# Kernel optimization log

Measured on AMD Instinct MI355X. Metric: run time of the kernel, lower is better.

The kernel has to match this reference:

```python
import jax, jax.numpy as jnp
import numpy as np

N_NODES = 500_000
N_EDGES = 1_000_000
EMB = 64           # config.Model.embedding_size
F = 128            # config.Model.latency_feature_size
L = 8              # config.Latency.latency_feature_length
OP_CNT = 5000
SV_CNT = 2000
ST_CNT = 16
IN_DIM = 3 * EMB + L  # 200


def setup_inputs() -> dict:
    key = jax.random.key(0)
    ks = jax.random.split(key, 24)
    s = 0.02
    inp = {
        'operation_id': jax.random.randint(ks[0], (N_NODES,), 0, OP_CNT, dtype=jnp.int32),
        'service_id':   jax.random.randint(ks[1], (N_NODES,), 0, SV_CNT, dtype=jnp.int32),
        'status_id':    jax.random.randint(ks[2], (N_NODES,), 0, ST_CNT, dtype=jnp.int32),
        'latency_feat': jax.random.normal(ks[3], (N_NODES, L), dtype=jnp.float32),
        'edge_src':     jax.random.randint(ks[4], (N_EDGES,), 0, N_NODES, dtype=jnp.int32),
        'edge_dst':     jax.random.randint(ks[5], (N_EDGES,), 0, N_NODES, dtype=jnp.int32),
        'eps':          jax.random.normal(ks[6], (N_NODES, F), dtype=jnp.float32),
        # parameters (LevelEmbedding + TreeLSTMLatencyEncoder + TreeLSTMLatencyDecoder)
        'op_embed':      jax.random.normal(ks[7],  (OP_CNT, EMB), dtype=jnp.float32) * s,
        'service_embed': jax.random.normal(ks[8],  (SV_CNT, EMB), dtype=jnp.float32) * s,
        'status_embed':  jax.random.normal(ks[9],  (ST_CNT, EMB), dtype=jnp.float32) * s,
        'enc_W1': jax.random.normal(ks[10], (IN_DIM, F), dtype=jnp.float32) * s,
        'enc_b1': jnp.zeros((F,), dtype=jnp.float32),
        'enc_W2': jax.random.normal(ks[11], (F, 2 * F), dtype=jnp.float32) * s,
        'enc_b2': jnp.zeros((2 * F,), dtype=jnp.float32),
        'dec_Wself': jax.random.normal(ks[12], (F, F), dtype=jnp.float32) * s,
        'dec_Wagg':  jax.random.normal(ks[13], (F, F), dtype=jnp.float32) * s,
        'mu_W': jax.random.normal(ks[14], (F, L), dtype=jnp.float32) * s,
        'mu_b': jnp.zeros((L,), dtype=jnp.float32),
        'lv_W': jax.random.normal(ks[15], (F, L), dtype=jnp.float32) * s,
        'lv_b': jnp.zeros((L,), dtype=jnp.float32),
        'opwise_embed': jax.random.normal(ks[16], (OP_CNT + 1, 2 * L * L), dtype=jnp.float32) * s,
    }
    return inp


def reference(operation_id, service_id, status_id, latency_feat, edge_src, edge_dst, eps,
              op_embed, service_embed, status_embed,
              enc_W1, enc_b1, enc_W2, enc_b2,
              dec_Wself, dec_Wagg, mu_W, mu_b, lv_W, lv_b, opwise_embed):
    N = latency_feat.shape[0]
    # ---- LevelEmbedding: gathers + concat ----
    feats = jnp.concatenate([
        op_embed[operation_id],
        service_embed[service_id],
        status_embed[status_id],
        latency_feat,
    ], axis=-1)  # [N, 3*EMB + L]
    # ---- TreeLSTMLatencyEncoder ----
    h = jax.nn.relu(feats @ enc_W1 + enc_b1)
    y = h @ enc_W2 + enc_b2                       # [N, 2F]
    z_mu, z_lv = jnp.split(y, 2, axis=-1)
    z_lv = jnp.tanh(z_lv)
    z = z_mu + jnp.exp(0.5 * z_lv) * eps          # reparameterize, [N, F]
    # ---- TreeLSTM decoder (one child-sum message-passing step over edges) ----
    agg = jax.ops.segment_sum(z[edge_src], edge_dst, num_segments=N)  # scatter-reduce
    yd = jax.nn.relu(z @ dec_Wself + agg @ dec_Wagg)                  # [N, F]
    mu = yd @ mu_W + mu_b   # [N, L]
    lv = yd @ lv_W + lv_b   # [N, L]
    # op-wise output transform: per-node [1,L] @ [L,L]
    w = opwise_embed[operation_id].reshape(N, L, 2 * L)
    w_mu, w_lv = w[..., :L], w[..., L:]
    mu = jnp.einsum('nl,nlk->nk', mu, w_mu)
    lv = jnp.einsum('nl,nlk->nk', lv, w_lv)
    # ---- latency_loss: gaussian NLL + opid scatter aggregation ----
    label = latency_feat
    loss = (mu - label) ** 2 / (2.0 * jnp.exp(lv) + 1e-7) + 0.5 * lv  # [N, L]
    loss_node = jnp.mean(loss, axis=1)                                 # [N]
    op_loss = jax.ops.segment_sum(loss_node, operation_id, num_segments=OP_CNT)
    op_cnt = jax.ops.segment_sum(jnp.ones((N,), jnp.int32), operation_id, num_segments=OP_CNT)
    lat_loss = jnp.mean(loss_node)
    kl = -0.5 * jnp.mean(z_lv + 1.0 - jnp.exp(z_lv) - z_mu ** 2)
    total = lat_loss + kl
    return (total, op_loss, op_cnt)
```

## Files before the change

kernel.cpp:

```cpp
#include <hip/hip_runtime.h>
#include <math.h>

#define NN 500000
#define NE 1000000
#define OPC 5000
#define NBLK_SCAN 489
#define NBLK ((NN + 127) / 128)

typedef short short8 __attribute__((ext_vector_type(8)));
typedef float f32x4 __attribute__((ext_vector_type(4)));

static __device__ __forceinline__ short f2bf(float f) {
    unsigned u = __builtin_bit_cast(unsigned, f);
    u += 0x7fffu + ((u >> 16) & 1u);
    return (short)(u >> 16);
}
static __device__ __forceinline__ float bf2f(short s) {
    unsigned u = ((unsigned)(unsigned short)s) << 16;
    return __builtin_bit_cast(float, u);
}
static __device__ __forceinline__ short8 cvt8(float4 a, float4 b) {
    short8 r;
    r[0] = f2bf(a.x); r[1] = f2bf(a.y); r[2] = f2bf(a.z); r[3] = f2bf(a.w);
    r[4] = f2bf(b.x); r[5] = f2bf(b.y); r[6] = f2bf(b.z); r[7] = f2bf(b.w);
    return r;
}
static __device__ __forceinline__ short8 ldcvt(const float* p) {
    const float4* p4 = (const float4*)p;
    return cvt8(p4[0], p4[1]);
}

__global__ void prep_kernel(const float* __restrict__ W1, const float* __restrict__ W2,
                            const float* __restrict__ Wself, const float* __restrict__ Wagg,
                            const float* __restrict__ muW, const float* __restrict__ lvW,
                            short* __restrict__ W1f, short* __restrict__ W2f,
                            short* __restrict__ Wf0, short* __restrict__ Wf1,
                            short* __restrict__ HWf)
{
    int idx = blockIdx.x * 256 + threadIdx.x;
    int j = idx & 7, lane = (idx >> 3) & 63;
    int m = lane & 15, q = lane >> 4;
    {
        int s = idx >> 12, nf = (idx >> 9) & 7;
        int k = s * 32 + q * 8 + j, col = nf * 16 + m;
        W1f[idx] = (k < 200) ? f2bf(W1[k * 128 + col]) : (short)0;
    }
    {
        int s = idx >> 13, nf = (idx >> 9) & 15;
        int k = s * 32 + q * 8 + j, col = nf * 16 + m;
        W2f[idx] = f2bf(W2[k * 256 + col]);
    }
    if (idx < 16384) {
        int s = idx >> 12, nf = (idx >> 9) & 7;
        int k = s * 32 + q * 8 + j, col = nf * 16 + m;
        Wf0[idx] = f2bf(Wself[k * 128 + col]);
        Wf1[idx] = f2bf(Wagg[k * 128 + col]);
    }
    if (idx < 2048) {
        int k = (idx >> 9) * 32 + q * 8 + j;
        HWf[idx] = (m < 8) ? f2bf(muW[k * 8 + m]) : f2bf(lvW[k * 8 + (m - 8)]);
    }
}

__global__ __launch_bounds__(256, 4) void enc1_mfma(
    const int* __restrict__ op_id, const int* __restrict__ sv_id, const int* __restrict__ st_id,
    const float* __restrict__ lat,
    const float* __restrict__ opE, const float* __restrict__ svE, const float* __restrict__ stE,
    const short* __restrict__ W1f, const float* __restrict__ b1,
    short* __restrict__ h_bf)
{
    __shared__ __align__(16) short Hs[128 * 136];
    const int tid = threadIdx.x;
    const int lane = tid & 63, w = tid >> 6;
    const int m = lane & 15, q = lane >> 4;
    const int bbase = blockIdx.x * 128;
    const int wbase = bbase + w * 32;
    const bool wv = (wbase < NN);

    f32x4 acc[2][8];
    #pragma unroll
    for (int a2 = 0; a2 < 2; a2++)
        #pragma unroll
        for (int nf = 0; nf < 8; nf++) acc[a2][nf] = (f32x4)0.0f;

    if (wv) {
        const int n0 = wbase + m, n1 = wbase + 16 + m;
        const size_t op0 = (size_t)op_id[n0] * 64, op1 = (size_t)op_id[n1] * 64;
        const size_t sv0 = (size_t)sv_id[n0] * 64, sv1 = (size_t)sv_id[n1] * 64;
        const size_t st0 = (size_t)st_id[n0] * 64, st1 = (size_t)st_id[n1] * 64;

        #pragma unroll
        for (int s = 0; s < 7; s++) {
            short8 a0, a1;
            if (s < 2) {
                a0 = ldcvt(opE + op0 + s * 32 + q * 8);
                a1 = ldcvt(opE + op1 + s * 32 + q * 8);
            } else if (s < 4) {
                a0 = ldcvt(svE + sv0 + (s - 2) * 32 + q * 8);
                a1 = ldcvt(svE + sv1 + (s - 2) * 32 + q * 8);
            } else if (s < 6) {
                a0 = ldcvt(stE + st0 + (s - 4) * 32 + q * 8);
                a1 = ldcvt(stE + st1 + (s - 4) * 32 + q * 8);
            } else {
                if (q == 0) {
                    a0 = ldcvt(lat + (size_t)n0 * 8);
                    a1 = ldcvt(lat + (size_t)n1 * 8);
                } else {
                    #pragma unroll
                    for (int i = 0; i < 8; i++) { a0[i] = 0; a1[i] = 0; }
                }
            }
            #pragma unroll
            for (int nf = 0; nf < 8; nf++) {
                const short8 b = *(const short8*)(W1f + (s * 8 + nf) * 512 + lane * 8);
                acc[0][nf] = __builtin_amdgcn_mfma_f32_16x16x32_bf16(a0, b, acc[0][nf], 0, 0, 0);
                acc[1][nf] = __builtin_amdgcn_mfma_f32_16x16x32_bf16(a1, b, acc[1][nf], 0, 0, 0);
            }
        }
    }

    if (wv) {
        #pragma unroll
        for (int nf = 0; nf < 8; nf++) {
            int col = nf * 16 + m;
            float bb = b1[col];
            #pragma unroll
            for (int a2 = 0; a2 < 2; a2++)
                #pragma unroll
                for (int r = 0; r < 4; r++) {
                    int g = w * 32 + a2 * 16 + q * 4 + r;
                    Hs[g * 136 + col] = f2bf(fmaxf(acc[a2][nf][r] + bb, 0.0f));
                }
        }
    }
    __syncthreads();

    {
        int g = tid >> 1, cb = (tid & 1) * 64;
        int node = bbase + g;
        if (node < NN) {
            short8* dst = (short8*)(h_bf + (size_t)node * 128 + cb);
            const short8* src = (const short8*)&Hs[g * 136 + cb];
            #pragma unroll
            for (int i = 0; i < 8; i++) dst[i] = src[i];
        }
    }
}

__global__ __launch_bounds__(256, 4) void enc2_mfma(
    const short* __restrict__ h_bf, const short* __restrict__ W2f, const float* __restrict__ b2,
    const float* __restrict__ eps, short* __restrict__ z_bf, float* __restrict__ kl_sum)
{
    __shared__ __align__(16) int ldsI[64 * 132];
    const int tid = threadIdx.x;
    const int lane = tid & 63, w = tid >> 6;
    const int m = lane & 15, q = lane >> 4;
    const int bbase = blockIdx.x * 128;
    const int wbase = bbase + w * 32;
    const bool wv = (wbase < NN);

    f32x4 acc[2][16];
    #pragma unroll
    for (int a2 = 0; a2 < 2; a2++)
        #pragma unroll
        for (int nf = 0; nf < 16; nf++) acc[a2][nf] = (f32x4)0.0f;

    if (wv) {
        short8 a[2][4];
        #pragma unroll
        for (int s = 0; s < 4; s++) {
            a[0][s] = *(const short8*)(h_bf + (size_t)(wbase + m) * 128 + s * 32 + q * 8);
            a[1][s] = *(const short8*)(h_bf + (size_t)(wbase + 16 + m) * 128 + s * 32 + q * 8);
        }
        #pragma unroll
        for (int s = 0; s < 4; s++) {
            #pragma unroll
            for (int nf = 0; nf < 16; nf++) {
                const short8 b = *(const short8*)(W2f + (s * 16 + nf) * 512 + lane * 8);
                acc[0][nf] = __builtin_amdgcn_mfma_f32_16x16x32_bf16(a[0][s], b, acc[0][nf], 0, 0, 0);
                acc[1][nf] = __builtin_amdgcn_mfma_f32_16x16x32_bf16(a[1][s], b, acc[1][nf], 0, 0, 0);
            }
        }
    }

    float kll = 0.0f;
    #pragma unroll
    for (int a2 = 0; a2 < 2; a2++) {
        if (wv) {
            #pragma unroll
            for (int nf = 0; nf < 8; nf++) {
                int col = nf * 16 + m;
                float bm = b2[col], bl = b2[col + 128];
                #pragma unroll
                for (int r = 0; r < 4; r++) {
                    float mu = acc[a2][nf][r] + bm;
                    float lr = acc[a2][nf + 8][r] + bl;
                    float e2 = __expf(2.0f * lr);
                    float t  = 1.0f - 2.0f * __builtin_amdgcn_rcpf(e2 + 1.0f);
                    float s  = __expf(0.5f * t);
                    kll += t + 1.0f - s * s - mu * mu;
                    int pk = (int)(unsigned short)f2bf(mu)
                           | ((int)(unsigned short)f2bf(s) << 16);
                    ldsI[(w * 16 + q * 4 + r) * 132 + col] = pk;
                }
            }
        }
        __syncthreads();
        {
            int g = tid >> 2, cb = (tid & 3) * 32;
            int node = bbase + (g >> 4) * 32 + a2 * 16 + (g & 15);
            if (node < NN) {
                const float4* ep = (const float4*)(eps + (size_t)node * 128 + cb);
                const int4*   lp = (const int4*)&ldsI[g * 132 + cb];
                #pragma unroll
                for (int c = 0; c < 4; c++) {
                    int4 va = lp[c * 2], vb = lp[c * 2 + 1];
                    float4 ea = ep[c * 2], eb = ep[c * 2 + 1];
                    short8 o;
                    o[0] = f2bf(fmaf(bf2f((short)(va.x >> 16)), ea.x, bf2f((short)va.x)));
                    o[1] = f2bf(fmaf(bf2f((short)(va.y >> 16)), ea.y, bf2f((short)va.y)));
                    o[2] = f2bf(fmaf(bf2f((short)(va.z >> 16)), ea.z, bf2f((short)va.z)));
                    o[3] = f2bf(fmaf(bf2f((short)(va.w >> 16)), ea.w, bf2f((short)va.w)));
                    o[4] = f2bf(fmaf(bf2f((short)(vb.x >> 16)), eb.x, bf2f((short)vb.x)));
                    o[5] = f2bf(fmaf(bf2f((short)(vb.y >> 16)), eb.y, bf2f((short)vb.y)));
                    o[6] = f2bf(fmaf(bf2f((short)(vb.z >> 16)), eb.z, bf2f((short)vb.z)));
                    o[7] = f2bf(fmaf(bf2f((short)(vb.w >> 16)), eb.w, bf2f((short)vb.w)));
                    *(short8*)(z_bf + (size_t)node * 128 + cb + c * 8) = o;
                }
            }
        }
        __syncthreads();
    }
    #pragma unroll
    for (int off = 32; off > 0; off >>= 1) kll += __shfl_down(kll, off);
    if (lane == 0) atomicAdd(kl_sum, kll);
}

__global__ void hist_kernel(const int* __restrict__ edst, int* __restrict__ cnt)
{
    int e = blockIdx.x * 256 + threadIdx.x;
    if (e < NE) atomicAdd(&cnt[edst[e]], 1);
}

__global__ void scan1_kernel(const int* __restrict__ cnt, int* __restrict__ bsum)
{
    __shared__ int ls[256];
    int b = blockIdx.x, tid = threadIdx.x;
    int idx0 = b * 1024 + tid * 4;
    int s = 0;
    #pragma unroll
    for (int i = 0; i < 4; i++) { int idx = idx0 + i; if (idx < NN) s += cnt[idx]; }
    ls[tid] = s; __syncthreads();
    for (int off = 128; off > 0; off >>= 1) {
        if (tid < off) ls[tid] += ls[tid + off];
        __syncthreads();
    }
    if (tid == 0) bsum[b] = ls[0];
}

__global__ void scan2_kernel(int* __restrict__ bsum, int* __restrict__ rowstart)
{
    __shared__ int ls[512];
    int tid = threadIdx.x;
    int v = (tid < NBLK_SCAN) ? bsum[tid] : 0;
    ls[tid] = v; __syncthreads();
    for (int off = 1; off < 512; off <<= 1) {
        int t = 0;
        if (tid >= off) t = ls[tid - off];
        __syncthreads();
        ls[tid] += t;
        __syncthreads();
    }
    if (tid < NBLK_SCAN) bsum[tid] = (tid == 0) ? 0 : ls[tid - 1];
    if (tid == 0) rowstart[NN] = NE;
}

__global__ void scan3_kernel(const int* __restrict__ cnt, const int* __restrict__ bsum,
                             int* __restrict__ rowstart, int* __restrict__ cursor)
{
    __shared__ int ls[256];
    int b = blockIdx.x, tid = threadIdx.x;
    int idx0 = b * 1024 + tid * 4;
    int v[4]; int s = 0;
    #pragma unroll
    for (int i = 0; i < 4; i++) { int idx = idx0 + i; v[i] = (idx < NN) ? cnt[idx] : 0; s += v[i]; }
    ls[tid] = s; __syncthreads();
    for (int off = 1; off < 256; off <<= 1) {
        int t = 0;
        if (tid >= off) t = ls[tid - off];
        __syncthreads();
        ls[tid] += t;
        __syncthreads();
    }
    int ex = ls[tid] - s + bsum[b];
    #pragma unroll
    for (int i = 0; i < 4; i++) {
        int idx = idx0 + i;
        if (idx < NN) { rowstart[idx] = ex; cursor[idx] = ex; }
        ex += v[i];
    }
}

__global__ void fill_kernel(const int* __restrict__ esrc, const int* __restrict__ edst,
                            int* __restrict__ cursor, int* __restrict__ csr)
{
    int e = blockIdx.x * 256 + threadIdx.x;
    if (e < NE) {
        int pos = atomicAdd(&cursor[edst[e]], 1);
        csr[pos] = esrc[e];
    }
}

__global__ __launch_bounds__(256, 4) void dec_mfma(
    const short* __restrict__ z_bf, const int* __restrict__ rowstart, const int* __restrict__ csr,
    const short* __restrict__ Wf0, const short* __restrict__ Wf1, const short* __restrict__ HWf,
    const float* __restrict__ mub, const float* __restrict__ lvb,
    const float* __restrict__ opwise, const int* __restrict__ op_id,
    const float* __restrict__ lat,
    float* __restrict__ op_loss, float* __restrict__ op_cnt,
    float* __restrict__ loss_sum)
{
    __shared__ __align__(16) short regionA[128 * 128];
    float* mlv = (float*)regionA;

    const int tid = threadIdx.x;
    const int lane = tid & 63, w = tid >> 6;
    const int m = lane & 15, q = lane >> 4;
    const int bbase = blockIdx.x * 128;
    const int wbase = bbase + w * 32;
    const bool wv = (wbase < NN);

    {
        int nodeL = tid & 127, hh = tid >> 7;
        int n = bbase + nodeL;
        float a[64];
        #pragma unroll
        for (int i = 0; i < 64; i++) a[i] = 0.0f;
        if (n < NN) {
            int r0 = rowstart[n], r1 = rowstart[n + 1];
            for (int e = r0; e < r1; e++) {
                const short8* zp = (const short8*)(z_bf + (size_t)csr[e] * 128 + hh * 64);
                #pragma unroll
                for (int j = 0; j < 8; j++) {
                    short8 v = zp[j];
                    #pragma unroll
                    for (int i = 0; i < 8; i++) a[j * 8 + i] += bf2f(v[i]);
                }
            }
        }
        #pragma unroll
        for (int j = 0; j < 8; j++) {
            int slot = ((hh * 8 + j) ^ (nodeL & 7)) * 8;
            short8 o;
            #pragma unroll
            for (int i = 0; i < 8; i++) o[i] = f2bf(a[j * 8 + i]);
            *(short8*)&regionA[nodeL * 128 + slot] = o;
        }
    }
    __syncthreads();

    f32x4 acc[2][8];
    #pragma unroll
    for (int a2 = 0; a2 < 2; a2++)
        #pragma unroll
        for (int nf = 0; nf < 8; nf++) acc[a2][nf] = (f32x4)0.0f;

    f32x4 h0 = (f32x4)0.0f, h1 = (f32x4)0.0f;

    if (wv) {
        short8 az[2][4];
        #pragma unroll
        for (int s = 0; s < 4; s++) {
            az[0][s] = *(const short8*)(z_bf + (size_t)(wbase + m) * 128 + s * 32 + q * 8);
            az[1][s] = *(const short8*)(z_bf + (size_t)(wbase + 16 + m) * 128 + s * 32 + q * 8);
        }
        #pragma unroll
        for (int s = 0; s < 4; s++) {
            #pragma unroll
            for (int nf = 0; nf < 8; nf++) {
                const short8 b = *(const short8*)(Wf0 + (s * 8 + nf) * 512 + lane * 8);
                acc[0][nf] = __builtin_amdgcn_mfma_f32_16x16x32_bf16(az[0][s], b, acc[0][nf], 0, 0, 0);
                acc[1][nf] = __builtin_amdgcn_mfma_f32_16x16x32_bf16(az[1][s], b, acc[1][nf], 0, 0, 0);
            }
        }

        #pragma unroll
        for (int s = 0; s < 4; s++) {
            const int slot = ((4 * s + q) ^ (m & 7)) * 8;
            const short8 a0 = *(const short8*)&regionA[(w * 32 + m) * 128 + slot];
            const short8 a1 = *(const short8*)&regionA[(w * 32 + 16 + m) * 128 + slot];
            #pragma unroll
            for (int nf = 0; nf < 8; nf++) {
                const short8 b = *(const short8*)(Wf1 + (s * 8 + nf) * 512 + lane * 8);
                acc[0][nf] = __builtin_amdgcn_mfma_f32_16x16x32_bf16(a0, b, acc[0][nf], 0, 0, 0);
                acc[1][nf] = __builtin_amdgcn_mfma_f32_16x16x32_bf16(a1, b, acc[1][nf], 0, 0, 0);
            }
        }

        #pragma unroll
        for (int a2 = 0; a2 < 2; a2++)
            #pragma unroll
            for (int nf = 0; nf < 8; nf++) {
                int c = nf * 2 + (m >> 3);
                #pragma unroll
                for (int r = 0; r < 4; r++) {
                    int node = w * 32 + a2 * 16 + q * 4 + r;
                    regionA[node * 128 + ((c ^ (node & 7)) * 8) + (m & 7)] =
                        f2bf(fmaxf(acc[a2][nf][r], 0.0f));
                }
            }

        #pragma unroll
        for (int s2 = 0; s2 < 4; s2++) {
            const int slot = ((4 * s2 + q) ^ (m & 7)) * 8;
            short8 a0 = *(const short8*)&regionA[(w * 32 + m) * 128 + slot];
            short8 a1 = *(const short8*)&regionA[(w * 32 + 16 + m) * 128 + slot];
            short8 b  = *(const short8*)(HWf + s2 * 512 + lane * 8);
            h0 = __builtin_amdgcn_mfma_f32_16x16x32_bf16(a0, b, h0, 0, 0, 0);
            h1 = __builtin_amdgcn_mfma_f32_16x16x32_bf16(a1, b, h1, 0, 0, 0);
        }
    }
    __syncthreads();

    if (wv) {
        float hb = (m < 8) ? mub[m] : lvb[m - 8];
        #pragma unroll
        for (int r = 0; r < 4; r++) {
            mlv[(w * 32 + q * 4 + r) * 17 + m]      = h0[r] + hb;
            mlv[(w * 32 + 16 + q * 4 + r) * 17 + m] = h1[r] + hb;
        }
    }
    __syncthreads();

    float lsum = 0.0f;
    if (tid < 128 && bbase + tid < NN) {
        const int t = tid;
        const int n = bbase + t;
        const int op = op_id[n];
        const float4* w4 = (const float4*)(opwise + (size_t)op * 128);
        float mout[8], lout[8];
        #pragma unroll
        for (int k = 0; k < 8; k++) { mout[k] = 0.0f; lout[k] = 0.0f; }
        #pragma unroll
        for (int l = 0; l < 8; l++) {
            float mv = mlv[t * 17 + l];
            float vv = mlv[t * 17 + 8 + l];
            float4 a = w4[l * 4 + 0];
            float4 b = w4[l * 4 + 1];
            float4 c = w4[l * 4 + 2];
            float4 d = w4[l * 4 + 3];
            mout[0] = fmaf(mv, a.x, mout[0]); mout[1] = fmaf(mv, a.y, mout[1]);
            mout[2] = fmaf(mv, a.z, mout[2]); mout[3] = fmaf(mv, a.w, mout[3]);
            mout[4] = fmaf(mv, b.x, mout[4]); mout[5] = fmaf(mv, b.y, mout[5]);
            mout[6] = fmaf(mv, b.z, mout[6]); mout[7] = fmaf(mv, b.w, mout[7]);
            lout[0] = fmaf(vv, c.x, lout[0]); lout[1] = fmaf(vv, c.y, lout[1]);
            lout[2] = fmaf(vv, c.z, lout[2]); lout[3] = fmaf(vv, c.w, lout[3]);
            lout[4] = fmaf(vv, d.x, lout[4]); lout[5] = fmaf(vv, d.y, lout[5]);
            lout[6] = fmaf(vv, d.z, lout[6]); lout[7] = fmaf(vv, d.w, lout[7]);
        }
        const float4* lp = (const float4*)(lat + (size_t)n * 8);
        float4 lb0 = lp[0], lb1 = lp[1];
        float labels[8] = {lb0.x, lb0.y, lb0.z, lb0.w, lb1.x, lb1.y, lb1.z, lb1.w};
        float lnode = 0.0f;
        #pragma unroll
        for (int k = 0; k < 8; k++) {
            float diff = mout[k] - labels[k];
            lnode += diff * diff / (2.0f * expf(lout[k]) + 1e-7f) + 0.5f * lout[k];
        }
        lnode *= 0.125f;
        atomicAdd(&op_loss[op], lnode);
        atomicAdd(&op_cnt[op], 1.0f);
        lsum = lnode;
    }
    #pragma unroll
    for (int off = 32; off > 0; off >>= 1) lsum += __shfl_down(lsum, off);
    if (lane == 0) atomicAdd(loss_sum, lsum);
}

__global__ void final_kernel(const float* __restrict__ accum, float* __restrict__ out)
{
    out[0] = accum[1] / (float)NN - 0.5f * (accum[0] / (float)((size_t)NN * 128));
}

extern "C" void kernel_launch(void* const* d_in, const int* in_sizes, int n_in,
                              void* d_out, int out_size, void* d_ws, size_t ws_size,
                              hipStream_t stream) {
    const int*   op_id  = (const int*)  d_in[0];
    const int*   sv_id  = (const int*)  d_in[1];
    const int*   st_id  = (const int*)  d_in[2];
    const float* lat    = (const float*)d_in[3];
    const int*   esrc   = (const int*)  d_in[4];
    const int*   edst   = (const int*)  d_in[5];
    const float* eps    = (const float*)d_in[6];
    const float* opE    = (const float*)d_in[7];
    const float* svE    = (const float*)d_in[8];
    const float* stE    = (const float*)d_in[9];
    const float* W1     = (const float*)d_in[10];
    const float* b1     = (const float*)d_in[11];
    const float* W2     = (const float*)d_in[12];
    const float* b2     = (const float*)d_in[13];
    const float* Wself  = (const float*)d_in[14];
    const float* Wagg   = (const float*)d_in[15];
    const float* muW    = (const float*)d_in[16];
    const float* mub    = (const float*)d_in[17];
    const float* lvW    = (const float*)d_in[18];
    const float* lvb    = (const float*)d_in[19];
    const float* opwise = (const float*)d_in[20];

    char* wsb = (char*)d_ws;
    short* W1f      = (short*)(wsb + 0);
    short* W2f      = (short*)(wsb + 65536);
    short* Wf0      = (short*)(wsb + 131072);
    short* Wf1      = (short*)(wsb + 163840);
    short* HWf      = (short*)(wsb + 196608);
    float* accum    = (float*)(wsb + 204800);
    int*   cnt      = (int*)  (wsb + (4  << 20));
    int*   rowstart = (int*)  (wsb + (6  << 20));
    int*   cursor   = (int*)  (wsb + (9  << 20));
    int*   csr      = (int*)  (wsb + (12 << 20));
    int*   bsum     = (int*)  (wsb + (16 << 20));
    short* h_bf     = (short*)(wsb + (32  << 20));
    short* z_bf     = (short*)(wsb + (160ull << 20));
    float* out      = (float*)d_out;

    hipMemsetAsync(d_out, 0, (size_t)out_size * sizeof(float), stream);
    hipMemsetAsync(accum, 0, 2 * sizeof(float), stream);
    hipMemsetAsync(cnt, 0, (size_t)NN * sizeof(int), stream);

    prep_kernel<<<128, 256, 0, stream>>>(W1, W2, Wself, Wagg, muW, lvW,
                                         W1f, W2f, Wf0, Wf1, HWf);

    hist_kernel<<<(NE + 255) / 256, 256, 0, stream>>>(edst, cnt);
    scan1_kernel<<<NBLK_SCAN, 256, 0, stream>>>(cnt, bsum);
    scan2_kernel<<<1, 512, 0, stream>>>(bsum, rowstart);
    scan3_kernel<<<NBLK_SCAN, 256, 0, stream>>>(cnt, bsum, rowstart, cursor);
    fill_kernel<<<(NE + 255) / 256, 256, 0, stream>>>(esrc, edst, cursor, csr);

    enc1_mfma<<<NBLK, 256, 0, stream>>>(op_id, sv_id, st_id, lat, opE, svE, stE, W1f, b1, h_bf);
    enc2_mfma<<<NBLK, 256, 0, stream>>>(h_bf, W2f, b2, eps, z_bf, accum + 0);
    dec_mfma<<<NBLK, 256, 0, stream>>>(z_bf, rowstart, csr, Wf0, Wf1, HWf, mub, lvb,
                                       opwise, op_id, lat,
                                       out + 1, out + 1 + OPC, accum + 1);
    final_kernel<<<1, 1, 0, stream>>>(accum, out);
}
```

Before: 1.210 ms.

## Process 16-row halves sequentially and split gather across four lanes per node

The encoder and decoder MFMA loops now handle the two 16-row sub-tiles one at a time instead of keeping both accumulator sets live. This roughly halves accumulator and A-fragment register pressure. The edge-gather aggregation now uses four threads per node with 32-float accumulators instead of two threads with 64, run in two passes over the 128 nodes. The aim is fewer VGPRs, possibly higher occupancy, and more parallel gather loads. In exchange, each weight B fragment is loaded twice, once per half, instead of being reused across both sub-tiles.

```diff
diff --git a/kernel.cpp b/kernel.cpp
--- a/kernel.cpp
+++ b/kernel.cpp
@@ -77,60 +77,47 @@
     const int wbase = bbase + w * 32;
     const bool wv = (wbase < NN);
 
-    f32x4 acc[2][8];
-    #pragma unroll
-    for (int a2 = 0; a2 < 2; a2++)
-        #pragma unroll
-        for (int nf = 0; nf < 8; nf++) acc[a2][nf] = (f32x4)0.0f;
-
-    if (wv) {
-        const int n0 = wbase + m, n1 = wbase + 16 + m;
-        const size_t op0 = (size_t)op_id[n0] * 64, op1 = (size_t)op_id[n1] * 64;
-        const size_t sv0 = (size_t)sv_id[n0] * 64, sv1 = (size_t)sv_id[n1] * 64;
-        const size_t st0 = (size_t)st_id[n0] * 64, st1 = (size_t)st_id[n1] * 64;
-
-        #pragma unroll
-        for (int s = 0; s < 7; s++) {
-            short8 a0, a1;
-            if (s < 2) {
-                a0 = ldcvt(opE + op0 + s * 32 + q * 8);
-                a1 = ldcvt(opE + op1 + s * 32 + q * 8);
-            } else if (s < 4) {
-                a0 = ldcvt(svE + sv0 + (s - 2) * 32 + q * 8);
-                a1 = ldcvt(svE + sv1 + (s - 2) * 32 + q * 8);
-            } else if (s < 6) {
-                a0 = ldcvt(stE + st0 + (s - 4) * 32 + q * 8);
-                a1 = ldcvt(stE + st1 + (s - 4) * 32 + q * 8);
-            } else {
-                if (q == 0) {
-                    a0 = ldcvt(lat + (size_t)n0 * 8);
-                    a1 = ldcvt(lat + (size_t)n1 * 8);
-                } else {
-                    #pragma unroll
-                    for (int i = 0; i < 8; i++) { a0[i] = 0; a1[i] = 0; }
+    #pragma unroll
+    for (int a2 = 0; a2 < 2; a2++) {
+        if (wv) {
+            const int n0 = wbase + a2 * 16 + m;
+            const size_t op0 = (size_t)op_id[n0] * 64;
+            const size_t sv0 = (size_t)sv_id[n0] * 64;
+            const size_t st0 = (size_t)st_id[n0] * 64;
+
+            f32x4 acc[8];
+            #pragma unroll
+            for (int nf = 0; nf < 8; nf++) acc[nf] = (f32x4)0.0f;
+
+            #pragma unroll
+            for (int s = 0; s < 7; s++) {
+                short8 a0;
+                if (s < 2)      a0 = ldcvt(opE + op0 + s * 32 + q * 8);
+                else if (s < 4) a0 = ldcvt(svE + sv0 + (s - 2) * 32 + q * 8);
+                else if (s < 6) a0 = ldcvt(stE + st0 + (s - 4) * 32 + q * 8);
+                else {
+                    if (q == 0) a0 = ldcvt(lat + (size_t)n0 * 8);
+                    else {
+                        #pragma unroll
+                        for (int i = 0; i < 8; i++) a0[i] = 0;
+                    }
+                }
+                #pragma unroll
+                for (int nf = 0; nf < 8; nf++) {
+                    const short8 b = *(const short8*)(W1f + (s * 8 + nf) * 512 + lane * 8);
+                    acc[nf] = __builtin_amdgcn_mfma_f32_16x16x32_bf16(a0, b, acc[nf], 0, 0, 0);
                 }
             }
             #pragma unroll
             for (int nf = 0; nf < 8; nf++) {
-                const short8 b = *(const short8*)(W1f + (s * 8 + nf) * 512 + lane * 8);
-                acc[0][nf] = __builtin_amdgcn_mfma_f32_16x16x32_bf16(a0, b, acc[0][nf], 0, 0, 0);
-                acc[1][nf] = __builtin_amdgcn_mfma_f32_16x16x32_bf16(a1, b, acc[1][nf], 0, 0, 0);
-            }
-        }
-    }
-
-    if (wv) {
-        #pragma unroll
-        for (int nf = 0; nf < 8; nf++) {
-            int col = nf * 16 + m;
-            float bb = b1[col];
-            #pragma unroll
-            for (int a2 = 0; a2 < 2; a2++)
+                int col = nf * 16 + m;
+                float bb = b1[col];
                 #pragma unroll
                 for (int r = 0; r < 4; r++) {
                     int g = w * 32 + a2 * 16 + q * 4 + r;
-                    Hs[g * 136 + col] = f2bf(fmaxf(acc[a2][nf][r] + bb, 0.0f));
-                }
+                    Hs[g * 136 + col] = f2bf(fmaxf(acc[nf][r] + bb, 0.0f));
+                }
+            }
         }
     }
     __syncthreads();
@@ -159,42 +146,36 @@
     const int wbase = bbase + w * 32;
     const bool wv = (wbase < NN);
 
-    f32x4 acc[2][16];
-    #pragma unroll
-    for (int a2 = 0; a2 < 2; a2++)
-        #pragma unroll
-        for (int nf = 0; nf < 16; nf++) acc[a2][nf] = (f32x4)0.0f;
-
-    if (wv) {
-        short8 a[2][4];
-        #pragma unroll
-        for (int s = 0; s < 4; s++) {
-            a[0][s] = *(const short8*)(h_bf + (size_t)(wbase + m) * 128 + s * 32 + q * 8);
-            a[1][s] = *(const short8*)(h_bf + (size_t)(wbase + 16 + m) * 128 + s * 32 + q * 8);
-        }
-        #pragma unroll
-        for (int s = 0; s < 4; s++) {
-            #pragma unroll
-            for (int nf = 0; nf < 16; nf++) {
-                const short8 b = *(const short8*)(W2f + (s * 16 + nf) * 512 + lane * 8);
-                acc[0][nf] = __builtin_amdgcn_mfma_f32_16x16x32_bf16(a[0][s], b, acc[0][nf], 0, 0, 0);
-                acc[1][nf] = __builtin_amdgcn_mfma_f32_16x16x32_bf16(a[1][s], b, acc[1][nf], 0, 0, 0);
-            }
-        }
-    }
-
     float kll = 0.0f;
     #pragma unroll
     for (int a2 = 0; a2 < 2; a2++) {
         if (wv) {
+            short8 a[4];
+            #pragma unroll
+            for (int s = 0; s < 4; s++)
+                a[s] = *(const short8*)(h_bf + (size_t)(wbase + a2 * 16 + m) * 128 + s * 32 + q * 8);
+
+            f32x4 acc[16];
+            #pragma unroll
+            for (int nf = 0; nf < 16; nf++) acc[nf] = (f32x4)0.0f;
+
+            #pragma unroll
+            for (int s = 0; s < 4; s++) {
+                #pragma unroll
+                for (int nf = 0; nf < 16; nf++) {
+                    const short8 b = *(const short8*)(W2f + (s * 16 + nf) * 512 + lane * 8);
+                    acc[nf] = __builtin_amdgcn_mfma_f32_16x16x32_bf16(a[s], b, acc[nf], 0, 0, 0);
+                }
+            }
+
             #pragma unroll
             for (int nf = 0; nf < 8; nf++) {
                 int col = nf * 16 + m;
                 float bm = b2[col], bl = b2[col + 128];
                 #pragma unroll
                 for (int r = 0; r < 4; r++) {
-                    float mu = acc[a2][nf][r] + bm;
-                    float lr = acc[a2][nf + 8][r] + bl;
+                    float mu = acc[nf][r] + bm;
+                    float lr = acc[nf + 8][r] + bl;
                     float e2 = __expf(2.0f * lr);
                     float t  = 1.0f - 2.0f * __builtin_amdgcn_rcpf(e2 + 1.0f);
                     float s  = __expf(0.5f * t);
@@ -330,18 +311,20 @@
     const int wbase = bbase + w * 32;
     const bool wv = (wbase < NN);
 
-    {
-        int nodeL = tid & 127, hh = tid >> 7;
+    #pragma unroll
+    for (int half = 0; half < 2; half++) {
+        int nodeL = half * 64 + (tid >> 2);
+        int chunk = tid & 3;
         int n = bbase + nodeL;
-        float a[64];
-        #pragma unroll
-        for (int i = 0; i < 64; i++) a[i] = 0.0f;
+        float a[32];
+        #pragma unroll
+        for (int i = 0; i < 32; i++) a[i] = 0.0f;
         if (n < NN) {
             int r0 = rowstart[n], r1 = rowstart[n + 1];
             for (int e = r0; e < r1; e++) {
-                const short8* zp = (const short8*)(z_bf + (size_t)csr[e] * 128 + hh * 64);
-                #pragma unroll
-                for (int j = 0; j < 8; j++) {
+                const short8* zp = (const short8*)(z_bf + (size_t)csr[e] * 128 + chunk * 32);
+                #pragma unroll
+                for (int j = 0; j < 4; j++) {
                     short8 v = zp[j];
                     #pragma unroll
                     for (int i = 0; i < 8; i++) a[j * 8 + i] += bf2f(v[i]);
@@ -349,8 +332,9 @@
             }
         }
         #pragma unroll
-        for (int j = 0; j < 8; j++) {
-            int slot = ((hh * 8 + j) ^ (nodeL & 7)) * 8;
+        for (int j = 0; j < 4; j++) {
+            int c = chunk * 4 + j;
+            int slot = (c ^ (nodeL & 7)) * 8;
             short8 o;
             #pragma unroll
             for (int i = 0; i < 8; i++) o[i] = f2bf(a[j * 8 + i]);
@@ -359,46 +343,41 @@
     }
     __syncthreads();
 
-    f32x4 acc[2][8];
-    #pragma unroll
-    for (int a2 = 0; a2 < 2; a2++)
-        #pragma unroll
-        for (int nf = 0; nf < 8; nf++) acc[a2][nf] = (f32x4)0.0f;
-
-    f32x4 h0 = (f32x4)0.0f, h1 = (f32x4)0.0f;
+    f32x4 h0[2];
+    h0[0] = (f32x4)0.0f; h0[1] = (f32x4)0.0f;
 
     if (wv) {
-        short8 az[2][4];
-        #pragma unroll
-        for (int s = 0; s < 4; s++) {
-            az[0][s] = *(const short8*)(z_bf + (size_t)(wbase + m) * 128 + s * 32 + q * 8);
-            az[1][s] = *(const short8*)(z_bf + (size_t)(wbase + 16 + m) * 128 + s * 32 + q * 8);
-        }
-        #pragma unroll
-        for (int s = 0; s < 4; s++) {
-            #pragma unroll
-            for (int nf = 0; nf < 8; nf++) {
-                const short8 b = *(const short8*)(Wf0 + (s * 8 + nf) * 512 + lane * 8);
-                acc[0][nf] = __builtin_amdgcn_mfma_f32_16x16x32_bf16(az[0][s], b, acc[0][nf], 0, 0, 0);
-                acc[1][nf] = __builtin_amdgcn_mfma_f32_16x16x32_bf16(az[1][s], b, acc[1][nf], 0, 0, 0);
-            }
-        }
-
-        #pragma unroll
-        for (int s = 0; s < 4; s++) {
-            const int slot = ((4 * s + q) ^ (m & 7)) * 8;
-            const short8 a0 = *(const short8*)&regionA[(w * 32 + m) * 128 + slot];
-            const short8 a1 = *(const short8*)&regionA[(w * 32 + 16 + m) * 128 + slot];
-            #pragma unroll
-            for (int nf = 0; nf < 8; nf++) {
-                const short8 b = *(const short8*)(Wf1 + (s * 8 + nf) * 512 + lane * 8);
-                acc[0][nf] = __builtin_amdgcn_mfma_f32_16x16x32_bf16(a0, b, acc[0][nf], 0, 0, 0);
-                acc[1][nf] = __builtin_amdgcn_mfma_f32_16x16x32_bf16(a1, b, acc[1][nf], 0, 0, 0);
-            }
-        }
-
-        #pragma unroll
-        for (int a2 = 0; a2 < 2; a2++)
+        #pragma unroll
+        for (int a2 = 0; a2 < 2; a2++) {
+            short8 az[4];
+            #pragma unroll
+            for (int s = 0; s < 4; s++)
+                az[s] = *(const short8*)(z_bf + (size_t)(wbase + a2 * 16 + m) * 128 + s * 32 + q * 8);
+
+            f32x4 acc[8];
+            #pragma unroll
+            for (int nf = 0; nf < 8; nf++) acc[nf] = (f32x4)0.0f;
+
+            #pragma unroll
+            for (int s = 0; s < 4; s++) {
+                #pragma unroll
+                for (int nf = 0; nf < 8; nf++) {
+                    const short8 b = *(const short8*)(Wf0 + (s * 8 + nf) * 512 + lane * 8);
+                    acc[nf] = __builtin_amdgcn_mfma_f32_16x16x32_bf16(az[s], b, acc[nf], 0, 0, 0);
+                }
+            }
+
+            #pragma unroll
+            for (int s = 0; s < 4; s++) {
+                const int slot = ((4 * s + q) ^ (m & 7)) * 8;
+                const short8 a0 = *(const short8*)&regionA[(w * 32 + a2 * 16 + m) * 128 + slot];
+                #pragma unroll
+                for (int nf = 0; nf < 8; nf++) {
+                    const short8 b = *(const short8*)(Wf1 + (s * 8 + nf) * 512 + lane * 8);
+                    acc[nf] = __builtin_amdgcn_mfma_f32_16x16x32_bf16(a0, b, acc[nf], 0, 0, 0);
+                }
+            }
+
             #pragma unroll
             for (int nf = 0; nf < 8; nf++) {
                 int c = nf * 2 + (m >> 3);
@@ -406,18 +385,17 @@
                 for (int r = 0; r < 4; r++) {
                     int node = w * 32 + a2 * 16 + q * 4 + r;
                     regionA[node * 128 + ((c ^ (node & 7)) * 8) + (m & 7)] =
-                        f2bf(fmaxf(acc[a2][nf][r], 0.0f));
-                }
-            }
-
-        #pragma unroll
-        for (int s2 = 0; s2 < 4; s2++) {
-            const int slot = ((4 * s2 + q) ^ (m & 7)) * 8;
-            short8 a0 = *(const short8*)&regionA[(w * 32 + m) * 128 + slot];
-            short8 a1 = *(const short8*)&regionA[(w * 32 + 16 + m) * 128 + slot];
-            short8 b  = *(const short8*)(HWf + s2 * 512 + lane * 8);
-            h0 = __builtin_amdgcn_mfma_f32_16x16x32_bf16(a0, b, h0, 0, 0, 0);
-            h1 = __builtin_amdgcn_mfma_f32_16x16x32_bf16(a1, b, h1, 0, 0, 0);
+                        f2bf(fmaxf(acc[nf][r], 0.0f));
+                }
+            }
+
+            #pragma unroll
+            for (int s2 = 0; s2 < 4; s2++) {
+                const int slot = ((4 * s2 + q) ^ (m & 7)) * 8;
+                short8 a0 = *(const short8*)&regionA[(w * 32 + a2 * 16 + m) * 128 + slot];
+                short8 b  = *(const short8*)(HWf + s2 * 512 + lane * 8);
+                h0[a2] = __builtin_amdgcn_mfma_f32_16x16x32_bf16(a0, b, h0[a2], 0, 0, 0);
+            }
         }
     }
     __syncthreads();
@@ -425,10 +403,10 @@
     if (wv) {
         float hb = (m < 8) ? mub[m] : lvb[m - 8];
         #pragma unroll
-        for (int r = 0; r < 4; r++) {
-            mlv[(w * 32 + q * 4 + r) * 17 + m]      = h0[r] + hb;
-            mlv[(w * 32 + 16 + q * 4 + r) * 17 + m] = h1[r] + hb;
-        }
+        for (int a2 = 0; a2 < 2; a2++)
+            #pragma unroll
+            for (int r = 0; r < 4; r++)
+                mlv[(w * 32 + a2 * 16 + q * 4 + r) * 17 + m] = h0[a2][r] + hb;
     }
     __syncthreads();
 
```

New measurement: 1.196 ms. No clear change (-1.2%).
